# Kernel optimization log

Hardware: AMD Instinct MI355X
Metric: run time of the kernel (lower is better)

## Reference

```python
import jax, jax.numpy as jnp
import numpy as np

EMBED = 1024
HEADS = 16
HEAD_DIM = EMBED // HEADS
B, S = 4, 1024


def setup_inputs() -> dict:
    key = jax.random.key(0)
    ks = jax.random.split(key, 8)
    return {
        "values": jax.random.normal(ks[0], (B, S, EMBED), dtype=jnp.float32),
        "keys": jax.random.normal(ks[1], (B, S, EMBED), dtype=jnp.float32),
        "query": jax.random.normal(ks[2], (B, S, EMBED), dtype=jnp.float32),
        "mask": jax.random.randint(ks[3], (B, 1, S, S), 0, 2, dtype=jnp.int32),
        "Wv": jax.random.normal(ks[4], (HEAD_DIM, HEAD_DIM), dtype=jnp.float32) / np.sqrt(HEAD_DIM),
        "Wq": jax.random.normal(ks[5], (HEAD_DIM, HEAD_DIM), dtype=jnp.float32) / np.sqrt(HEAD_DIM),
        "Wk": jax.random.normal(ks[6], (HEAD_DIM, HEAD_DIM), dtype=jnp.float32) / np.sqrt(HEAD_DIM),
        "Wu": jax.random.normal(ks[7], (EMBED, EMBED), dtype=jnp.float32) / np.sqrt(EMBED),
        "bu": jnp.zeros((EMBED,), dtype=jnp.float32),
    }


def reference(values, keys, query, mask, Wv, Wq, Wk, Wu, bu):
    n, s, _ = query.shape
    # split heads: [B, S, H, D]
    v = values.reshape(n, s, HEADS, HEAD_DIM)
    k = keys.reshape(n, s, HEADS, HEAD_DIM)
    q = query.reshape(n, s, HEADS, HEAD_DIM)
    # per-head linear (shared weight across heads); torch Linear: x @ W.T
    v = jnp.einsum("nshd,ed->nshe", v, Wv)
    k = jnp.einsum("nshd,ed->nshe", k, Wk)
    q = jnp.einsum("nshd,ed->nshe", q, Wq)
    # scores: [B, H, Q, K]
    dot = jnp.einsum("nqhd,nkhd->nhqk", q, k)
    dot = jnp.where(mask == 0, jnp.float32(-1e20), dot)
    # NOTE: original scales by sqrt(embed_size), not sqrt(head_dim)
    attn = jax.nn.softmax(dot / jnp.sqrt(jnp.float32(EMBED)), axis=3)
    out = jnp.einsum("nhql,nlhd->nqhd", attn, v)
    out = out.reshape(n, s, EMBED)
    return out @ Wu.T + bu
```

## Files before the change

kernel.cpp:

```cpp
#include <hip/hip_runtime.h>
#include <hip/hip_bf16.h>

#define EMBED 1024
#define HEADS 16
#define HDIM  64
#define BATCH 4
#define SEQ   1024

typedef __attribute__((ext_vector_type(8))) short  short8;
typedef __attribute__((ext_vector_type(4))) short  short4v;
typedef __attribute__((ext_vector_type(4))) float  float4v;
typedef __attribute__((ext_vector_type(8))) float  float8;
typedef __attribute__((ext_vector_type(2))) __bf16 bf16x2;
typedef __attribute__((ext_vector_type(8))) __bf16 bf16x8;

static __device__ __forceinline__ short cvt1(float f) {
  return __builtin_bit_cast(short, (__bf16)f);
}

static __device__ __forceinline__ unsigned pkbf(float a, float b) {
  bf16x2 v; v[0] = (__bf16)a; v[1] = (__bf16)b;
  return __builtin_bit_cast(unsigned, v);
}

static __device__ __forceinline__ float ex2(float x) {
  return __builtin_amdgcn_exp2f(x);
}

static __device__ __forceinline__ short8 cvt8(const float* p) {
  float4v a = *(const float4v*)p;
  float4v b = *(const float4v*)(p + 4);
  float8 f = __builtin_shufflevector(a, b, 0, 1, 2, 3, 4, 5, 6, 7);
  bf16x8 bb = __builtin_convertvector(f, bf16x8);
  return __builtin_bit_cast(short8, bb);
}

static __device__ __forceinline__ void block_sync_lds() {
  __builtin_amdgcn_sched_barrier(0);
  asm volatile("s_waitcnt lgkmcnt(0)" ::: "memory");
  __builtin_amdgcn_s_barrier();
  __builtin_amdgcn_sched_barrier(0);
}

#define QSCL 0.04508422002778011f

__global__ __launch_bounds__(256) void k_pre(
    const float* __restrict__ values, const float* __restrict__ keys,
    const float* __restrict__ query,
    const float* __restrict__ Wv, const float* __restrict__ Wq,
    const float* __restrict__ Wk, const float* __restrict__ Wu,
    const int* __restrict__ mask,
    short* __restrict__ qp, short* __restrict__ kp, short* __restrict__ vpT,
    unsigned char* __restrict__ maskb, short* __restrict__ wub) {
  const int b = blockIdx.x;
  const int t = threadIdx.x;
  if (b < 768) {
    const int l = t & 63, lr = l & 15, g = l >> 4;
    const int wbase = (b * 4 + (t >> 6)) * 4;
    const int z = wbase >> 12;
    const float* in_; const float* Wm;
    if (z == 0)      { in_ = query;  Wm = Wq; }
    else if (z == 1) { in_ = keys;   Wm = Wk; }
    else             { in_ = values; Wm = Wv; }
    const float scl = (z == 0) ? QSCL : 1.0f;

    short8 af0[4], af1[4];
    int hh[4], rr[4];
#pragma unroll
    for (int uu = 0; uu < 4; ++uu) {
      const int rem = (wbase + uu) & 4095;
      hh[uu] = rem & 15;
      rr[uu] = (rem >> 4) * 16;
      af0[uu] = cvt8(in_ + (size_t)(rr[uu] + lr) * EMBED + hh[uu] * HDIM + g * 8);
      af1[uu] = cvt8(in_ + (size_t)(rr[uu] + lr) * EMBED + hh[uu] * HDIM + 32 + g * 8);
    }
    short8 wf0[4], wf1[4];
#pragma unroll
    for (int nt = 0; nt < 4; ++nt) {
      wf0[nt] = cvt8(Wm + (size_t)(nt * 16 + lr) * HDIM + g * 8);
      wf1[nt] = cvt8(Wm + (size_t)(nt * 16 + lr) * HDIM + 32 + g * 8);
    }

#pragma unroll
    for (int uu = 0; uu < 4; ++uu) {
      const int h = hh[uu], r0 = rr[uu];
      const int n = r0 >> 10, s0 = r0 & 1023;
      const int nh = n * HEADS + h;
      float4v acc[4];
#pragma unroll
      for (int nt = 0; nt < 4; ++nt) {
        acc[nt] = (float4v){0.f, 0.f, 0.f, 0.f};
        acc[nt] = __builtin_amdgcn_mfma_f32_16x16x32_bf16(af0[uu], wf0[nt], acc[nt], 0, 0, 0);
        acc[nt] = __builtin_amdgcn_mfma_f32_16x16x32_bf16(af1[uu], wf1[nt], acc[nt], 0, 0, 0);
      }
      if (z == 2) {
#pragma unroll
        for (int nt = 0; nt < 4; ++nt) {
          short4v r;
          r[0]=cvt1(acc[nt][0]); r[1]=cvt1(acc[nt][1]);
          r[2]=cvt1(acc[nt][2]); r[3]=cvt1(acc[nt][3]);
          *(short4v*)(vpT + (size_t)(nh * HDIM + nt * 16 + lr) * SEQ + s0 + g * 4) = r;
        }
      } else {
        short* outp = (z == 0) ? qp : kp;
        const int b8 = ((s0 >> 4) & 1) * 8;
        const int rbase = s0 & ~31;
#pragma unroll
        for (int nt = 0; nt < 4; ++nt)
#pragma unroll
          for (int i = 0; i < 4; ++i) {
            const int row = (z == 0)
                ? (s0 + g * 4 + i)
                : (rbase + (g & 1) * 16 + b8 + (g >> 1) * 4 + i);
            outp[(size_t)(nh * SEQ + row) * HDIM + nt * 16 + lr] =
                cvt1(acc[nt][i] * scl);
          }
      }
    }
  } else if (b < 1280) {
    const int q0 = ((b - 768) * 8) * 256 + t;
#pragma unroll
    for (int it = 0; it < 8; ++it) {
      const int q = q0 + it * 256;
      uint4 v = *(const uint4*)(mask + (size_t)q * 4);
      unsigned nib = (v.x ? 1u : 0u) | (v.y ? 2u : 0u) |
                     (v.z ? 4u : 0u) | (v.w ? 8u : 0u);
      maskb[q] = (unsigned char)nib;
    }
  } else {
    const int base = (b - 1280) * 256 + t;
#pragma unroll
    for (int it = 0; it < 16; ++it) {
      int i4 = (base + it * 16384) * 4;
      float4v v = *(const float4v*)(Wu + i4);
      short4v r; r[0]=cvt1(v[0]); r[1]=cvt1(v[1]); r[2]=cvt1(v[2]); r[3]=cvt1(v[3]);
      *(short4v*)(wub + i4) = r;
    }
  }
}

__global__ __launch_bounds__(256, 2) void k_attn(
    const short* __restrict__ qp, const short* __restrict__ kp,
    const short* __restrict__ vpT, const unsigned char* __restrict__ maskb,
    short* __restrict__ ao) {
  const int bid = blockIdx.x;
  const int work = (bid & 7) * 64 + (bid >> 3);
  const int qt = work & 7, grp = work >> 3;
  const int h = grp & 15, n = grp >> 4;

  const int t256 = threadIdx.x;
  const int w = t256 >> 6, l = t256 & 63, lr = l & 15, g = l >> 4;
  const int nh = n * HEADS + h;
  const int q00 = qt * 128 + w * 16;
  const short* qb  = qp  + (size_t)nh * SEQ * HDIM;
  const short* kbp = kp  + (size_t)nh * SEQ * HDIM;
  const short* vb  = vpT + (size_t)nh * HDIM * SEQ;
  const unsigned char* mb0 = maskb + (size_t)(n * SEQ + q00 + lr) * 256;

  __shared__ __align__(16) short kls0[4096], kls1[4096];
  __shared__ __align__(16) short vls0[4096], vls1[4096];

  const int s0 = t256, s1 = t256 + 256;
  const int r0s = s0 >> 3, c0s = s0 & 7, r1s = s1 >> 3, c1s = s1 & 7;
  const int ld0 = r0s * 64 + ((c0s ^ (r0s & 7)) << 3);
  const int ld1 = r1s * 64 + ((c1s ^ (r1s & 7)) << 3);

  const int e = lr & 7;
  const int base0 = lr * 64 + ((g ^ e) << 3);
  const int base1 = lr * 64 + (((4 + g) ^ e) << 3);

  short8 qf0[2], qf1[2];
#pragma unroll
  for (int x = 0; x < 2; ++x) {
    qf0[x] = *(const short8*)(qb + (q00 + x * 64 + lr) * HDIM + g * 8);
    qf1[x] = *(const short8*)(qb + (q00 + x * 64 + lr) * HDIM + 32 + g * 8);
  }

  const short8 ones8 = {0x3F80, 0x3F80, 0x3F80, 0x3F80,
                        0x3F80, 0x3F80, 0x3F80, 0x3F80};

  float4v acc[2][4];
  float4v lac[2];
#pragma unroll
  for (int x = 0; x < 2; ++x) {
    lac[x] = (float4v){0.f, 0.f, 0.f, 0.f};
#pragma unroll
    for (int dt = 0; dt < 4; ++dt) acc[x][dt] = (float4v){0.f, 0.f, 0.f, 0.f};
  }

  auto issue = [&](int tile, short8& K0, short8& K1, short8& V0, short8& V1) {
    const int kn = tile * 64;
    K0 = *(const short8*)(kbp + kn * 64 + s0 * 8);
    K1 = *(const short8*)(kbp + kn * 64 + s1 * 8);
    V0 = *(const short8*)(vb + (size_t)r0s * SEQ + kn + c0s * 8);
    V1 = *(const short8*)(vb + (size_t)r1s * SEQ + kn + c1s * 8);
  };
  auto publish = [&](short* Kd, short* Vd, short8 K0, short8 K1, short8 V0, short8 V1) {
    *(short8*)(Kd + ld0) = K0;
    *(short8*)(Kd + ld1) = K1;
    *(short8*)(Vd + ld0) = V0;
    *(short8*)(Vd + ld1) = V1;
  };
  auto tilec = [&](const short* Kb, const short* Vb, int t) {
    float4v sT[2][4];
#pragma unroll
    for (int a = 0; a < 4; ++a) {
      short8 kf0 = *(const short8*)(Kb + a * 1024 + base0);
      short8 kf1 = *(const short8*)(Kb + a * 1024 + base1);
#pragma unroll
      for (int x = 0; x < 2; ++x) {
        float4v z = (float4v){0.f, 0.f, 0.f, 0.f};
        z = __builtin_amdgcn_mfma_f32_16x16x32_bf16(kf0, qf0[x], z, 0, 0, 0);
        sT[x][a] = __builtin_amdgcn_mfma_f32_16x16x32_bf16(kf1, qf1[x], z, 0, 0, 0);
      }
    }
    short8 pw0[2], pw1[2];
#pragma unroll
    for (int x = 0; x < 2; ++x) {
      uint4 mv = *(const uint4*)(mb0 + (size_t)x * 64 * 256 + t * 16);
      const unsigned wl = (g & 2) ? mv.y : mv.x;
      const unsigned wh = (g & 2) ? mv.w : mv.z;
      const int sh = (g & 1) * 16;
      unsigned dw[8];
#pragma unroll
      for (int a = 0; a < 4; ++a) {
        unsigned ta = ((a & 2) ? wh : wl) >> (sh + (a & 1) * 8);
        float p0 = ex2(sT[x][a][0]); p0 = (ta & 1u) ? p0 : 0.f;
        float p1 = ex2(sT[x][a][1]); p1 = (ta & 2u) ? p1 : 0.f;
        float p2 = ex2(sT[x][a][2]); p2 = (ta & 4u) ? p2 : 0.f;
        float p3 = ex2(sT[x][a][3]); p3 = (ta & 8u) ? p3 : 0.f;
        dw[a * 2]     = pkbf(p0, p1);
        dw[a * 2 + 1] = pkbf(p2, p3);
      }
      __builtin_memcpy(&pw0[x], &dw[0], 16);
      __builtin_memcpy(&pw1[x], &dw[4], 16);
      lac[x] = __builtin_amdgcn_mfma_f32_16x16x32_bf16(ones8, pw0[x], lac[x], 0, 0, 0);
      lac[x] = __builtin_amdgcn_mfma_f32_16x16x32_bf16(ones8, pw1[x], lac[x], 0, 0, 0);
    }
#pragma unroll
    for (int dt = 0; dt < 4; ++dt) {
      short8 vf0 = *(const short8*)(Vb + dt * 1024 + base0);
      short8 vf1 = *(const short8*)(Vb + dt * 1024 + base1);
#pragma unroll
      for (int x = 0; x < 2; ++x) {
        acc[x][dt] = __builtin_amdgcn_mfma_f32_16x16x32_bf16(vf0, pw0[x], acc[x][dt], 0, 0, 0);
        acc[x][dt] = __builtin_amdgcn_mfma_f32_16x16x32_bf16(vf1, pw1[x], acc[x][dt], 0, 0, 0);
      }
    }
  };

  short8 aK0, aK1, aV0, aV1;
  short8 bK0, bK1, bV0, bV1;

  issue(0, aK0, aK1, aV0, aV1);
  publish(kls0, vls0, aK0, aK1, aV0, aV1);
  issue(1, bK0, bK1, bV0, bV1);
  block_sync_lds();

  for (int tp = 0; tp < 8; ++tp) {
    if (tp < 7) issue(2 * tp + 2, aK0, aK1, aV0, aV1);
    tilec(kls0, vls0, 2 * tp);
    publish(kls1, vls1, bK0, bK1, bV0, bV1);
    block_sync_lds();
    if (tp < 7) issue(2 * tp + 3, bK0, bK1, bV0, bV1);
    tilec(kls1, vls1, 2 * tp + 1);
    if (tp < 7) {
      publish(kls0, vls0, aK0, aK1, aV0, aV1);
      block_sync_lds();
    }
  }

#pragma unroll
  for (int x = 0; x < 2; ++x) {
    const float inv = 1.f / fmaxf(lac[x][0], 1e-35f);
    short* aorow = ao + (size_t)(n * SEQ + q00 + x * 64 + lr) * EMBED + h * HDIM;
#pragma unroll
    for (int dt = 0; dt < 4; ++dt) {
      short4v r;
      r[0] = cvt1(acc[x][dt][0] * inv);
      r[1] = cvt1(acc[x][dt][1] * inv);
      r[2] = cvt1(acc[x][dt][2] * inv);
      r[3] = cvt1(acc[x][dt][3] * inv);
      *(short4v*)(aorow + dt * 16 + g * 4) = r;
    }
  }
}

__global__ __launch_bounds__(512, 1) void k_gemm(
    const short* __restrict__ ao, const short* __restrict__ wub,
    const float* __restrict__ bu, float* __restrict__ out) {
  const int r0 = blockIdx.x * 128, c0 = blockIdx.y * 128;
  const int t = threadIdx.x;
  const int w = t >> 6, l = t & 63, lr = l & 15, g = l >> 4;
  const int wr = w >> 2, wc = w & 3;

  __shared__ __align__(16) short als[2][128 * 64];
  __shared__ __align__(16) short bls[2][128 * 64];

  const int ar0 = t >> 3, ac0 = t & 7;
  const int ar1 = (t + 512) >> 3, ac1 = (t + 512) & 7;
  const int ld0 = ar0 * 64 + ((ac0 ^ (ar0 & 7)) << 3);
  const int ld1 = ar1 * 64 + ((ac1 ^ (ar1 & 7)) << 3);
  const short* agp0 = ao  + (size_t)(r0 + ar0) * EMBED + ac0 * 8;
  const short* agp1 = ao  + (size_t)(r0 + ar1) * EMBED + ac1 * 8;
  const short* bgp0 = wub + (size_t)(c0 + ar0) * EMBED + ac0 * 8;
  const short* bgp1 = wub + (size_t)(c0 + ar1) * EMBED + ac1 * 8;

  int aoff[4][2], boff[2][2];
#pragma unroll
  for (int fr = 0; fr < 4; ++fr) {
    const int ra = wr * 64 + fr * 16 + lr;
#pragma unroll
    for (int kk = 0; kk < 2; ++kk)
      aoff[fr][kk] = ra * 64 + (((kk * 4 + g) ^ (ra & 7)) << 3);
  }
#pragma unroll
  for (int fc = 0; fc < 2; ++fc) {
    const int rb = wc * 32 + fc * 16 + lr;
#pragma unroll
    for (int kk = 0; kk < 2; ++kk)
      boff[fc][kk] = rb * 64 + (((kk * 4 + g) ^ (rb & 7)) << 3);
  }

  float4v acc[4][2];
#pragma unroll
  for (int fr = 0; fr < 4; ++fr)
#pragma unroll
    for (int fc = 0; fc < 2; ++fc) acc[fr][fc] = (float4v){0.f, 0.f, 0.f, 0.f};

  {
    short8 a0 = *(const short8*)agp0;
    short8 a1 = *(const short8*)agp1;
    short8 b0 = *(const short8*)bgp0;
    short8 b1 = *(const short8*)bgp1;
    *(short8*)(&als[0][0] + ld0) = a0;
    *(short8*)(&als[0][0] + ld1) = a1;
    *(short8*)(&bls[0][0] + ld0) = b0;
    *(short8*)(&bls[0][0] + ld1) = b1;
  }
  block_sync_lds();

#pragma unroll 2
  for (int tt = 0; tt < 16; ++tt) {
    const int cur = tt & 1, nxt = cur ^ 1;
    short8 sA0, sA1, sB0, sB1;
    if (tt < 15) {
      const int kb = (tt + 1) * 64;
      sA0 = *(const short8*)(agp0 + kb);
      sA1 = *(const short8*)(agp1 + kb);
      sB0 = *(const short8*)(bgp0 + kb);
      sB1 = *(const short8*)(bgp1 + kb);
    }
#pragma unroll
    for (int kk = 0; kk < 2; ++kk) {
      short8 bf0 = *(const short8*)(&bls[cur][0] + boff[0][kk]);
      short8 bf1 = *(const short8*)(&bls[cur][0] + boff[1][kk]);
#pragma unroll
      for (int fr = 0; fr < 4; ++fr) {
        short8 af = *(const short8*)(&als[cur][0] + aoff[fr][kk]);
        acc[fr][0] = __builtin_amdgcn_mfma_f32_16x16x32_bf16(af, bf0, acc[fr][0], 0, 0, 0);
        acc[fr][1] = __builtin_amdgcn_mfma_f32_16x16x32_bf16(af, bf1, acc[fr][1], 0, 0, 0);
      }
    }
    if (tt < 15) {
      *(short8*)(&als[nxt][0] + ld0) = sA0;
      *(short8*)(&als[nxt][0] + ld1) = sA1;
      *(short8*)(&bls[nxt][0] + ld0) = sB0;
      *(short8*)(&bls[nxt][0] + ld1) = sB1;
      block_sync_lds();
    }
  }

#pragma unroll
  for (int fc = 0; fc < 2; ++fc) {
    const int col = c0 + wc * 32 + fc * 16 + lr;
    const float bv = bu[col];
#pragma unroll
    for (int fr = 0; fr < 4; ++fr)
#pragma unroll
      for (int i = 0; i < 4; ++i) {
        const int row = r0 + wr * 64 + fr * 16 + g * 4 + i;
        out[(size_t)row * EMBED + col] = acc[fr][fc][i] + bv;
      }
  }
}

extern "C" void kernel_launch(void* const* d_in, const int* in_sizes, int n_in,
                              void* d_out, int out_size, void* d_ws, size_t ws_size,
                              hipStream_t stream) {
  const float* values = (const float*)d_in[0];
  const float* keys   = (const float*)d_in[1];
  const float* query  = (const float*)d_in[2];
  const int*   mask   = (const int*)d_in[3];
  const float* Wv     = (const float*)d_in[4];
  const float* Wq     = (const float*)d_in[5];
  const float* Wk     = (const float*)d_in[6];
  const float* Wu     = (const float*)d_in[7];
  const float* bu     = (const float*)d_in[8];
  float* out = (float*)d_out;

  char* ws = (char*)d_ws;
  short* qp  = (short*)ws;
  short* kp  = qp + (1u << 22);
  short* vpT = kp + (1u << 22);
  short* ao  = vpT + (1u << 22);
  unsigned char* maskb = (unsigned char*)(ws + (32u << 20));
  short* wub = (short*)(ws + (36u << 20));

  k_pre<<<dim3(1344), 256, 0, stream>>>(values, keys, query, Wv, Wq, Wk, Wu,
                                        mask, qp, kp, vpT, maskb, wub);
  k_attn<<<dim3(512), 256, 0, stream>>>(qp, kp, vpT, maskb, ao);
  k_gemm<<<dim3(32, 8), 512, 0, stream>>>(ao, wub, bu, out);
}
```

Before: 76.25 us.

## Halve output-GEMM waves with larger per-wave tiles and two-stage register prefetch

The output projection GEMM now runs 256 threads instead of 512. Each wave computes a 64x64 tile (4x4 MFMA fragments) instead of 64x32, so each A fragment read from LDS is reused across four B fragments. Global loads are issued two K-steps ahead into two alternating register sets, with LDS double-buffered, to hide more memory latency. The cost is higher register pressure and fewer waves per CU to hide latency.

```diff
diff --git a/kernel.cpp b/kernel.cpp
--- a/kernel.cpp
+++ b/kernel.cpp
@@ -286,27 +286,29 @@
   }
 }
 
-__global__ __launch_bounds__(512, 1) void k_gemm(
+__global__ __launch_bounds__(256, 1) void k_gemm(
     const short* __restrict__ ao, const short* __restrict__ wub,
     const float* __restrict__ bu, float* __restrict__ out) {
   const int r0 = blockIdx.x * 128, c0 = blockIdx.y * 128;
   const int t = threadIdx.x;
   const int w = t >> 6, l = t & 63, lr = l & 15, g = l >> 4;
-  const int wr = w >> 2, wc = w & 3;
+  const int wr = w >> 1, wc = w & 1;
 
   __shared__ __align__(16) short als[2][128 * 64];
   __shared__ __align__(16) short bls[2][128 * 64];
 
-  const int ar0 = t >> 3, ac0 = t & 7;
-  const int ar1 = (t + 512) >> 3, ac1 = (t + 512) & 7;
-  const int ld0 = ar0 * 64 + ((ac0 ^ (ar0 & 7)) << 3);
-  const int ld1 = ar1 * 64 + ((ac1 ^ (ar1 & 7)) << 3);
-  const short* agp0 = ao  + (size_t)(r0 + ar0) * EMBED + ac0 * 8;
-  const short* agp1 = ao  + (size_t)(r0 + ar1) * EMBED + ac1 * 8;
-  const short* bgp0 = wub + (size_t)(c0 + ar0) * EMBED + ac0 * 8;
-  const short* bgp1 = wub + (size_t)(c0 + ar1) * EMBED + ac1 * 8;
-
-  int aoff[4][2], boff[2][2];
+  int ldc[4];
+  const short *agp[4], *bgp[4];
+#pragma unroll
+  for (int j = 0; j < 4; ++j) {
+    const int c = t + 256 * j;
+    const int row = c >> 3, c8 = c & 7;
+    ldc[j] = row * 64 + ((c8 ^ (row & 7)) << 3);
+    agp[j] = ao  + (size_t)(r0 + row) * EMBED + c8 * 8;
+    bgp[j] = wub + (size_t)(c0 + row) * EMBED + c8 * 8;
+  }
+
+  int aoff[4][2], boff[4][2];
 #pragma unroll
   for (int fr = 0; fr < 4; ++fr) {
     const int ra = wr * 64 + fr * 16 + lr;
@@ -315,65 +317,74 @@
       aoff[fr][kk] = ra * 64 + (((kk * 4 + g) ^ (ra & 7)) << 3);
   }
 #pragma unroll
-  for (int fc = 0; fc < 2; ++fc) {
-    const int rb = wc * 32 + fc * 16 + lr;
+  for (int fc = 0; fc < 4; ++fc) {
+    const int rb = wc * 64 + fc * 16 + lr;
 #pragma unroll
     for (int kk = 0; kk < 2; ++kk)
       boff[fc][kk] = rb * 64 + (((kk * 4 + g) ^ (rb & 7)) << 3);
   }
 
-  float4v acc[4][2];
+  float4v acc[4][4];
 #pragma unroll
   for (int fr = 0; fr < 4; ++fr)
 #pragma unroll
-    for (int fc = 0; fc < 2; ++fc) acc[fr][fc] = (float4v){0.f, 0.f, 0.f, 0.f};
-
-  {
-    short8 a0 = *(const short8*)agp0;
-    short8 a1 = *(const short8*)agp1;
-    short8 b0 = *(const short8*)bgp0;
-    short8 b1 = *(const short8*)bgp1;
-    *(short8*)(&als[0][0] + ld0) = a0;
-    *(short8*)(&als[0][0] + ld1) = a1;
-    *(short8*)(&bls[0][0] + ld0) = b0;
-    *(short8*)(&bls[0][0] + ld1) = b1;
-  }
+    for (int fc = 0; fc < 4; ++fc) acc[fr][fc] = (float4v){0.f, 0.f, 0.f, 0.f};
+
+  short8 sAa[4], sBa[4], sAb[4], sBb[4];
+
+  auto issueg = [&](int step, short8* SA, short8* SB) {
+    const int kb = step * 64;
+#pragma unroll
+    for (int j = 0; j < 4; ++j) {
+      SA[j] = *(const short8*)(agp[j] + kb);
+      SB[j] = *(const short8*)(bgp[j] + kb);
+    }
+  };
+  auto publishg = [&](short* Ad, short* Bd, const short8* SA, const short8* SB) {
+#pragma unroll
+    for (int j = 0; j < 4; ++j) {
+      *(short8*)(Ad + ldc[j]) = SA[j];
+      *(short8*)(Bd + ldc[j]) = SB[j];
+    }
+  };
+  auto stepc = [&](const short* Ab, const short* Bb) {
+#pragma unroll
+    for (int kk = 0; kk < 2; ++kk) {
+      short8 bf[4];
+#pragma unroll
+      for (int fc = 0; fc < 4; ++fc)
+        bf[fc] = *(const short8*)(Bb + boff[fc][kk]);
+#pragma unroll
+      for (int fr = 0; fr < 4; ++fr) {
+        short8 af = *(const short8*)(Ab + aoff[fr][kk]);
+#pragma unroll
+        for (int fc = 0; fc < 4; ++fc)
+          acc[fr][fc] = __builtin_amdgcn_mfma_f32_16x16x32_bf16(af, bf[fc], acc[fr][fc], 0, 0, 0);
+      }
+    }
+  };
+
+  issueg(0, sAa, sBa);
+  publishg(&als[0][0], &bls[0][0], sAa, sBa);
+  issueg(1, sAb, sBb);
   block_sync_lds();
 
-#pragma unroll 2
-  for (int tt = 0; tt < 16; ++tt) {
-    const int cur = tt & 1, nxt = cur ^ 1;
-    short8 sA0, sA1, sB0, sB1;
-    if (tt < 15) {
-      const int kb = (tt + 1) * 64;
-      sA0 = *(const short8*)(agp0 + kb);
-      sA1 = *(const short8*)(agp1 + kb);
-      sB0 = *(const short8*)(bgp0 + kb);
-      sB1 = *(const short8*)(bgp1 + kb);
-    }
-#pragma unroll
-    for (int kk = 0; kk < 2; ++kk) {
-      short8 bf0 = *(const short8*)(&bls[cur][0] + boff[0][kk]);
-      short8 bf1 = *(const short8*)(&bls[cur][0] + boff[1][kk]);
-#pragma unroll
-      for (int fr = 0; fr < 4; ++fr) {
-        short8 af = *(const short8*)(&als[cur][0] + aoff[fr][kk]);
-        acc[fr][0] = __builtin_amdgcn_mfma_f32_16x16x32_bf16(af, bf0, acc[fr][0], 0, 0, 0);
-        acc[fr][1] = __builtin_amdgcn_mfma_f32_16x16x32_bf16(af, bf1, acc[fr][1], 0, 0, 0);
-      }
-    }
-    if (tt < 15) {
-      *(short8*)(&als[nxt][0] + ld0) = sA0;
-      *(short8*)(&als[nxt][0] + ld1) = sA1;
-      *(short8*)(&bls[nxt][0] + ld0) = sB0;
-      *(short8*)(&bls[nxt][0] + ld1) = sB1;
+  for (int tp = 0; tp < 8; ++tp) {
+    if (tp < 7) issueg(2 * tp + 2, sAa, sBa);
+    stepc(&als[0][0], &bls[0][0]);
+    publishg(&als[1][0], &bls[1][0], sAb, sBb);
+    block_sync_lds();
+    if (tp < 7) issueg(2 * tp + 3, sAb, sBb);
+    stepc(&als[1][0], &bls[1][0]);
+    if (tp < 7) {
+      publishg(&als[0][0], &bls[0][0], sAa, sBa);
       block_sync_lds();
     }
   }
 
 #pragma unroll
-  for (int fc = 0; fc < 2; ++fc) {
-    const int col = c0 + wc * 32 + fc * 16 + lr;
+  for (int fc = 0; fc < 4; ++fc) {
+    const int col = c0 + wc * 64 + fc * 16 + lr;
     const float bv = bu[col];
 #pragma unroll
     for (int fr = 0; fr < 4; ++fr)
@@ -410,5 +421,5 @@
   k_pre<<<dim3(1344), 256, 0, stream>>>(values, keys, query, Wv, Wq, Wk, Wu,
                                         mask, qp, kp, vpT, maskb, wub);
   k_attn<<<dim3(512), 256, 0, stream>>>(qp, kp, vpT, maskb, ao);
-  k_gemm<<<dim3(32, 8), 512, 0, stream>>>(ao, wub, bu, out);
-}
+  k_gemm<<<dim3(32, 8), 256, 0, stream>>>(ao, wub, bu, out);
+}
```

New measurement: 74.15 us (median of 2 runs). 2.8% less time.
